# Performance work log

Measured on AMD Instinct MI355X. Metric: run time of the kernel, lower is better.

## Reference

```python
import jax, jax.numpy as jnp
import numpy as np

D_MODEL = 1024
N_HEADS = 16
HEAD_DIM = D_MODEL // N_HEADS
FFN = 4096
NUM_REL = 64
BATCH = 4
SEQ = 1024
EPS = 1e-6


def _layernorm(x, g, b):
    mu = jnp.mean(x, axis=-1, keepdims=True)
    var = jnp.mean(jnp.square(x - mu), axis=-1, keepdims=True)
    return (x - mu) * jax.lax.rsqrt(var + EPS) * g + b


def setup_inputs() -> dict:
    key = jax.random.key(0)
    ks = jax.random.split(key, 16)
    s_d = 1.0 / np.sqrt(D_MODEL)
    s_f = 1.0 / np.sqrt(FFN)
    inp = {
        "x": jax.random.normal(ks[0], (BATCH, SEQ, D_MODEL), jnp.float32),
        "relative_ids": jax.random.randint(ks[1], (SEQ, SEQ), 0, NUM_REL),
        # attention projections (row-major: y = x @ W + b)
        "Wq": jax.random.normal(ks[2], (D_MODEL, D_MODEL), jnp.float32) * s_d,
        "bq": jnp.zeros((D_MODEL,), jnp.float32),
        "Wk": jax.random.normal(ks[3], (D_MODEL, D_MODEL), jnp.float32) * s_d,
        "bk": jnp.zeros((D_MODEL,), jnp.float32),
        "Wv": jax.random.normal(ks[4], (D_MODEL, D_MODEL), jnp.float32) * s_d,
        "bv": jnp.zeros((D_MODEL,), jnp.float32),
        "Wo": jax.random.normal(ks[5], (D_MODEL, D_MODEL), jnp.float32) * s_d,
        "bo": jnp.zeros((D_MODEL,), jnp.float32),
        # relative position tables: Ek for keys (rel-e), Eb per-head bias (rel-b)
        "Ek": jax.random.normal(ks[6], (NUM_REL, HEAD_DIM), jnp.float32) * (1.0 / np.sqrt(HEAD_DIM)),
        "Eb": jax.random.normal(ks[7], (NUM_REL, N_HEADS), jnp.float32) * 0.02,
        # layernorms
        "g1": jnp.ones((D_MODEL,), jnp.float32),
        "b1": jnp.zeros((D_MODEL,), jnp.float32),
        "g2": jnp.ones((D_MODEL,), jnp.float32),
        "b2": jnp.zeros((D_MODEL,), jnp.float32),
        # FFN
        "W1": jax.random.normal(ks[8], (D_MODEL, FFN), jnp.float32) * s_d,
        "bf1": jnp.zeros((FFN,), jnp.float32),
        "W2": jax.random.normal(ks[9], (FFN, D_MODEL), jnp.float32) * s_f,
        "bf2": jnp.zeros((D_MODEL,), jnp.float32),
    }
    return inp


def _forward(x, relative_ids, Wq, bq, Wk, bk, Wv, bv, Wo, bo, Ek, Eb,
             g1, b1, g2, b2, W1, bf1, W2, bf2):
    B, S, D = x.shape
    # projections -> [B, H, S, Dh]
    def split_heads(t):
        return t.reshape(B, S, N_HEADS, HEAD_DIM).transpose(0, 2, 1, 3)
    q = split_heads(x @ Wq + bq)
    k = split_heads(x @ Wk + bk)
    v = split_heads(x @ Wv + bv)

    scores = jnp.einsum('bhqd,bhkd->bhqk', q, k)
    # rel-e: relative key embeddings interact with queries
    Erel = Ek[relative_ids]                      # [S, S, Dh]
    scores = scores + jnp.einsum('bhqd,qkd->bhqk', q, Erel)
    # rel-b: per-head relative bias
    scores = scores + Eb[relative_ids].transpose(2, 0, 1)[None]  # [1,H,S,S]
    scores = scores / jnp.sqrt(jnp.asarray(HEAD_DIM, x.dtype))

    attn = jax.nn.softmax(scores, axis=-1)
    ctx = jnp.einsum('bhqk,bhkd->bhqd', attn, v)
    ctx = ctx.transpose(0, 2, 1, 3).reshape(B, S, D)
    a_out = ctx @ Wo + bo

    # dropout is identity at eval
    ff_in = _layernorm(x + a_out, g1, b1)
    ff = jax.nn.relu(ff_in @ W1 + bf1) @ W2 + bf2
    return _layernorm(ff_in + ff, g2, b2)


def reference(x, relative_ids, Wq, bq, Wk, bk, Wv, bv, Wo, bo, Ek, Eb,
              g1, b1, g2, b2, W1, bf1, W2, bf2):
    return _forward(x, relative_ids, Wq, bq, Wk, bk, Wv, bv, Wo, bo, Ek, Eb,
                    g1, b1, g2, b2, W1, bf1, W2, bf2)
```

## Files before the change

### kernel.cpp

```cpp
#include <hip/hip_runtime.h>


typedef short bf16x8 __attribute__((ext_vector_type(8)));
typedef float f32x4 __attribute__((ext_vector_type(4)));

#define DEVI static __device__ __forceinline__

constexpr int SEQ = 1024, DMODEL = 1024, NH = 16, HDIM = 64, FFDIM = 4096, NREL = 64, NBATCH = 4;
constexpr int ROWS = NBATCH * SEQ;
#define QSC 0.18033688011112042f
#define MAXC 16.0f

DEVI unsigned short f2b(float f) {
  union { float f; unsigned u; } v; v.f = f;
  unsigned r = v.u + 0x7FFFu + ((v.u >> 16) & 1u);
  return (unsigned short)(r >> 16);
}

#if __has_builtin(__builtin_amdgcn_cvt_pk_bf16_f32)
DEVI unsigned pack2(float a, float b) {
  auto r = __builtin_amdgcn_cvt_pk_bf16_f32(a, b);
  return __builtin_bit_cast(unsigned, r);
}
#else
DEVI unsigned pack2(float a, float b) {
  return (unsigned)f2b(a) | ((unsigned)f2b(b) << 16);
}
#endif

DEVI float fexp2(float x) {
#if __has_builtin(__builtin_amdgcn_exp2f)
  return __builtin_amdgcn_exp2f(x);
#else
  return exp2f(x);
#endif
}

DEVI float4 ld4h(const unsigned short* p) {
  uint2 u = *(const uint2*)p;
  union { unsigned v; float f; } a, b, c, d;
  a.v = u.x << 16; b.v = u.x & 0xffff0000u; c.v = u.y << 16; d.v = u.y & 0xffff0000u;
  return make_float4(a.f, b.f, c.f, d.f);
}

DEVI void gload16(const unsigned short* g, unsigned short* l) {
  __builtin_amdgcn_global_load_lds((const __attribute__((address_space(1))) void*)g,
                                   (__attribute__((address_space(3))) void*)l, 16, 0, 0);
}

template <int BM, int BN, int WR, int WC>
DEVI void gemm_core(const unsigned short* __restrict__ A, int lda,
                    const unsigned short* __restrict__ Bt, int ldb, int K,
                    unsigned short* sA, unsigned short* sB, f32x4* acc) {
  constexpr int BK = 64;
  constexpr int MT = BM / (WR * 16), NT = BN / (WC * 16);
  const int tid = threadIdx.x;
  const int wave = tid >> 6, lane = tid & 63;
  const int wm = wave % WR, wn = wave / WR;
  const int lr = lane & 15, kq = lane >> 4;
  const int srow = lane >> 3;
  const int schunk = (lane & 7) ^ (srow & 7);
  const int sw = lr & 7;

  const f32x4 zero = {0.f, 0.f, 0.f, 0.f};
#pragma unroll
  for (int i = 0; i < MT * NT; ++i) acc[i] = zero;

  const unsigned short* ga = A + (size_t)(wave * (BM / 4) + srow) * lda + schunk * 8;
  const unsigned short* gb = Bt + (size_t)(wave * (BN / 4) + srow) * ldb + schunk * 8;
  unsigned short* la = sA + wave * (BM / 4) * BK;
  unsigned short* lb = sB + wave * (BN / 4) * BK;
  const unsigned short* pa = sA + (wm * MT * 16 + lr) * BK;
  const unsigned short* pb = sB + (wn * NT * 16 + lr) * BK;

  for (int k0 = 0; k0 < K; k0 += BK) {
#pragma unroll
    for (int j = 0; j < BM / 32; ++j) gload16(ga + (size_t)(j * 8) * lda + k0, la + j * 8 * BK);
#pragma unroll
    for (int j = 0; j < BN / 32; ++j) gload16(gb + (size_t)(j * 8) * ldb + k0, lb + j * 8 * BK);
    __syncthreads();
#pragma unroll
    for (int ks = 0; ks < 2; ++ks) {
      const int rc = ((ks * 4 + kq) ^ sw) * 8;
      bf16x8 af[MT], bv[NT];
#pragma unroll
      for (int mi = 0; mi < MT; ++mi) af[mi] = *(const bf16x8*)(pa + mi * 16 * BK + rc);
#pragma unroll
      for (int ni = 0; ni < NT; ++ni) bv[ni] = *(const bf16x8*)(pb + ni * 16 * BK + rc);
#pragma unroll
      for (int mi = 0; mi < MT; ++mi)
#pragma unroll
        for (int ni = 0; ni < NT; ++ni)
          acc[mi * NT + ni] =
              __builtin_amdgcn_mfma_f32_16x16x32_bf16(af[mi], bv[ni], acc[mi * NT + ni], 0, 0, 0);
    }
    __syncthreads();
  }
}

#define EPI_VARS                                     \
  const int tid = threadIdx.x;                       \
  const int wave = tid >> 6, lane = tid & 63;        \
  const int wm = wave % WR, wn = wave / WR;          \
  const int lr = lane & 15, kq = lane >> 4;

__global__ __launch_bounds__(256) void k_proj_qkv(
    const unsigned short* __restrict__ A, const unsigned short* __restrict__ WqT,
    const unsigned short* __restrict__ WkT, const unsigned short* __restrict__ WvT,
    const float* __restrict__ bq, const float* __restrict__ bk, const float* __restrict__ bv,
    unsigned short* __restrict__ oq, unsigned short* __restrict__ ok,
    unsigned short* __restrict__ ov) {
  constexpr int BM = 128, BN = 128, WR = 2, WC = 2, MT = 4, NT = 4;
  __shared__ __align__(16) unsigned short sA[BM * 64];
  __shared__ __align__(16) unsigned short sB[BN * 64];
  f32x4 acc[MT * NT];
  const int which = blockIdx.z;
  const unsigned short* Bt = which == 0 ? WqT : which == 1 ? WkT : WvT;
  const float* bias = which == 0 ? bq : which == 1 ? bk : bv;
  unsigned short* out = which == 0 ? oq : which == 1 ? ok : ov;
  const float scl = which == 0 ? QSC : 1.0f;
  const int m0 = blockIdx.y * BM, n0 = blockIdx.x * BN;
  gemm_core<BM, BN, WR, WC>(A + (size_t)m0 * DMODEL, DMODEL, Bt + (size_t)n0 * DMODEL, DMODEL,
                            DMODEL, sA, sB, acc);
  EPI_VARS
#pragma unroll
  for (int mi = 0; mi < MT; ++mi) {
    const int row0 = m0 + wm * MT * 16 + mi * 16 + kq * 4;
    const int b = row0 >> 10, s0 = row0 & 1023;
#pragma unroll
    for (int ni = 0; ni < NT; ++ni) {
      const int col = n0 + wn * NT * 16 + ni * 16 + lr;
      const int h = col >> 6, d = col & 63;
      const float bc = bias[col];
      f32x4 v = acc[mi * NT + ni];
#pragma unroll
      for (int r = 0; r < 4; ++r) v[r] = (v[r] + bc) * scl;
      if (which != 2) {
#pragma unroll
        for (int r = 0; r < 4; ++r)
          out[((size_t)((b * NH + h) * SEQ) + s0 + r) * HDIM + d] = f2b(v[r]);
      } else {
        uint2 p = make_uint2(pack2(v[0], v[1]), pack2(v[2], v[3]));
        *(uint2*)&out[((size_t)((b * NH + h) * HDIM) + d) * SEQ + s0] = p;
      }
    }
  }
}

template <int BM, int BN, int WR, int WC, bool RELU, bool OUTBF16, bool SPLITK = false>
__global__ __launch_bounds__(256) void k_gemm(const unsigned short* __restrict__ A, int lda,
                                              const unsigned short* __restrict__ Bt, int ldb, int K,
                                              int N, const float* __restrict__ bias,
                                              float* __restrict__ outf,
                                              unsigned short* __restrict__ outh,
                                              size_t ostride = 0) {
  constexpr int MT = BM / (WR * 16), NT = BN / (WC * 16);
  __shared__ __align__(16) unsigned short sA[BM * 64];
  __shared__ __align__(16) unsigned short sB[BN * 64];
  f32x4 acc[MT * NT];
  const int m0 = blockIdx.y * BM, n0 = blockIdx.x * BN;
  const int kc = SPLITK ? blockIdx.z : 0;
  gemm_core<BM, BN, WR, WC>(A + (size_t)m0 * lda + (size_t)kc * K, lda,
                            Bt + (size_t)n0 * ldb + (size_t)kc * K, ldb, K, sA, sB, acc);
  if (SPLITK) outh += (size_t)kc * ostride;
  EPI_VARS
#pragma unroll
  for (int mi = 0; mi < MT; ++mi) {
    const int row0 = m0 + wm * MT * 16 + mi * 16 + kq * 4;
#pragma unroll
    for (int ni = 0; ni < NT; ++ni) {
      const int col = n0 + wn * NT * 16 + ni * 16 + lr;
      const float bc = (bias && (!SPLITK || kc == 0)) ? bias[col] : 0.f;
      f32x4 v = acc[mi * NT + ni];
#pragma unroll
      for (int r = 0; r < 4; ++r) {
        float y = v[r] + bc;
        if (RELU) y = fmaxf(y, 0.f);
        if (OUTBF16 || SPLITK)
          outh[(size_t)(row0 + r) * N + col] = f2b(y);
        else
          outf[(size_t)(row0 + r) * N + col] = y;
      }
    }
  }
}

__global__ __launch_bounds__(256) void k_flash(const unsigned short* __restrict__ q,
                                               const unsigned short* __restrict__ kk,
                                               const unsigned short* __restrict__ vT,
                                               const unsigned short* __restrict__ Ekb,
                                               const float* __restrict__ Eb,
                                               const int* __restrict__ rel,
                                               unsigned short* __restrict__ ctx) {
  __shared__ __align__(16) unsigned short sK[128 * 64];
  __shared__ __align__(16) unsigned short sV[64 * 128];
  __shared__ __align__(16) float sqEB[64 * 68];
  __shared__ float sRow[4][16];

  const int tid = threadIdx.x, wave = tid >> 6, lane = tid & 63;
  const int lr = lane & 15, kq = lane >> 4;
  const int qt = blockIdx.x, z = blockIdx.y;
  const int b = z >> 4, h = z & 15;
  const size_t zo = (size_t)z * SEQ * HDIM;
  const size_t vo = (size_t)z * HDIM * SEQ;

  const int srow8 = lane >> 3, sl8 = lane & 7;
  const int sw8 = sl8 ^ (srow8 & 7);
  const int dl = lane >> 4, sl16 = lane & 15;
  const int swl = lr & 7;
  const f32x4 zero = {0.f, 0.f, 0.f, 0.f};

  unsigned short* sQv = sV;
#pragma unroll
  for (int j = 0; j < 2; ++j) {
    const int row = wave * 16 + j * 8 + srow8;
    gload16(q + zo + (size_t)(qt * 64 + row) * 64 + sw8 * 8, sQv + (wave * 16 + j * 8) * 64);
    gload16(Ekb + (size_t)row * 64 + sw8 * 8, sK + (wave * 16 + j * 8) * 64);
  }
  __syncthreads();

  bf16x8 bq_[2];
#pragma unroll
  for (int ks = 0; ks < 2; ++ks)
    bq_[ks] = *(const bf16x8*)&sQv[(wave * 16 + lr) * 64 + (((ks * 4 + kq) ^ swl) << 3)];

  {
    f32x4 accE[4];
#pragma unroll
    for (int nf = 0; nf < 4; ++nf) accE[nf] = zero;
#pragma unroll
    for (int ks = 0; ks < 2; ++ks) {
#pragma unroll
      for (int nf = 0; nf < 4; ++nf) {
        bf16x8 ek = *(const bf16x8*)&sK[(nf * 16 + lr) * 64 + (((ks * 4 + kq) ^ swl) << 3)];
        accE[nf] = __builtin_amdgcn_mfma_f32_16x16x32_bf16(bq_[ks], ek, accE[nf], 0, 0, 0);
      }
    }
#pragma unroll
    for (int nf = 0; nf < 4; ++nf) {
      const int rid = nf * 16 + lr;
      const float eb = Eb[rid * NH + h] * QSC - MAXC;
      f32x4 vv = accE[nf];
      vv[0] += eb; vv[1] += eb; vv[2] += eb; vv[3] += eb;
      *(f32x4*)&sqEB[rid * 68 + wave * 16 + kq * 4] = vv;
    }
  }

  float l_run = 0.f;
  f32x4 accO[4];
#pragma unroll
  for (int nd = 0; nd < 4; ++nd) accO[nd] = zero;
  const int qrow_g = qt * 64 + wave * 16 + lr;
  const int* relrow = rel + (size_t)qrow_g * SEQ;
  const int qcol = wave * 16 + lr;
  unsigned short* sPw = sK + wave * 2048;

  for (int kt = 0; kt < 8; ++kt) {
    __syncthreads();
#pragma unroll
    for (int j = 0; j < 4; ++j) {
      const int row = wave * 32 + j * 8 + srow8;
      gload16(kk + zo + (size_t)(kt * 128 + row) * 64 + sw8 * 8, sK + (wave * 32 + j * 8) * 64);
    }
#pragma unroll
    for (int j = 0; j < 4; ++j) {
      const int row = wave * 16 + j * 4 + dl;
      const int ch = sl16 ^ (row & 15);
      gload16(vT + vo + (size_t)row * SEQ + kt * 128 + ch * 8, sV + (wave * 16 + j * 4) * 128);
    }
    int4 r4[8];
#pragma unroll
    for (int mi = 0; mi < 8; ++mi) r4[mi] = *(const int4*)&relrow[kt * 128 + mi * 16 + kq * 4];
    __syncthreads();

    f32x4 accS[8];
#pragma unroll
    for (int mi = 0; mi < 8; ++mi) accS[mi] = zero;
#pragma unroll
    for (int ks = 0; ks < 2; ++ks) {
#pragma unroll
      for (int mi = 0; mi < 8; ++mi) {
        bf16x8 a = *(const bf16x8*)&sK[(mi * 16 + lr) * 64 + (((ks * 4 + kq) ^ swl) << 3)];
        accS[mi] = __builtin_amdgcn_mfma_f32_16x16x32_bf16(a, bq_[ks], accS[mi], 0, 0, 0);
      }
    }
#pragma unroll
    for (int mi = 0; mi < 8; ++mi) {
      const float p0 = fexp2(accS[mi][0] + sqEB[r4[mi].x * 68 + qcol]);
      const float p1 = fexp2(accS[mi][1] + sqEB[r4[mi].y * 68 + qcol]);
      const float p2 = fexp2(accS[mi][2] + sqEB[r4[mi].z * 68 + qcol]);
      const float p3 = fexp2(accS[mi][3] + sqEB[r4[mi].w * 68 + qcol]);
      accS[mi][0] = p0; accS[mi][1] = p1; accS[mi][2] = p2; accS[mi][3] = p3;
      l_run += (p0 + p1) + (p2 + p3);
    }
    __syncthreads();

#pragma unroll
    for (int mi = 0; mi < 8; ++mi) {
      const int c = 2 * mi + (kq >> 1);
      *(uint2*)&sPw[lr * 128 + ((c ^ lr) << 3) + ((kq & 1) << 2)] =
          make_uint2(pack2(accS[mi][0], accS[mi][1]), pack2(accS[mi][2], accS[mi][3]));
    }
#pragma unroll
    for (int kst = 0; kst < 4; ++kst) {
      const int cc = ((kq + 4 * kst) ^ lr) << 3;
      bf16x8 a = *(const bf16x8*)&sPw[lr * 128 + cc];
#pragma unroll
      for (int nd = 0; nd < 4; ++nd) {
        bf16x8 bv = *(const bf16x8*)&sV[(nd * 16 + lr) * 128 + cc];
        accO[nd] = __builtin_amdgcn_mfma_f32_16x16x32_bf16(a, bv, accO[nd], 0, 0, 0);
      }
    }
  }

  l_run += __shfl_xor(l_run, 16);
  l_run += __shfl_xor(l_run, 32);
  if (kq == 0) sRow[wave][lr] = l_run;
  const float4 lv = *(const float4*)&sRow[wave][kq * 4];
  const float inv[4] = {1.f / lv.x, 1.f / lv.y, 1.f / lv.z, 1.f / lv.w};
  const size_t rbase = (size_t)(b * SEQ + qt * 64 + wave * 16 + kq * 4);
#pragma unroll
  for (int nd = 0; nd < 4; ++nd) {
    const int col = h * HDIM + nd * 16 + lr;
#pragma unroll
    for (int r = 0; r < 4; ++r)
      ctx[(rbase + r) * DMODEL + col] = f2b(accO[nd][r] * inv[r]);
  }
}

template <bool WB>
__global__ __launch_bounds__(256) void k_addln3(const unsigned short* __restrict__ a,
                                                const unsigned short* __restrict__ p0,
                                                const unsigned short* __restrict__ p1,
                                                const float* __restrict__ g,
                                                const float* __restrict__ beta,
                                                float* __restrict__ outf,
                                                unsigned short* __restrict__ outh) {
  const int row = blockIdx.x, t = threadIdx.x;
  const size_t base = (size_t)row * DMODEL + t * 4;
  float4 va = ld4h(&a[base]);
  float4 v0 = ld4h(&p0[base]);
  float4 v1 = ld4h(&p1[base]);
  const float x0 = va.x + v0.x + v1.x, x1 = va.y + v0.y + v1.y;
  const float x2 = va.z + v0.z + v1.z, x3 = va.w + v0.w + v1.w;
  __shared__ float red[4];
  float s = x0 + x1 + x2 + x3;
#pragma unroll
  for (int o = 32; o; o >>= 1) s += __shfl_xor(s, o);
  if ((t & 63) == 0) red[t >> 6] = s;
  __syncthreads();
  const float mu = (red[0] + red[1] + red[2] + red[3]) * (1.0f / DMODEL);
  __syncthreads();
  const float d0 = x0 - mu, d1 = x1 - mu, d2 = x2 - mu, d3 = x3 - mu;
  float qv = d0 * d0 + d1 * d1 + d2 * d2 + d3 * d3;
#pragma unroll
  for (int o = 32; o; o >>= 1) qv += __shfl_xor(qv, o);
  if ((t & 63) == 0) red[t >> 6] = qv;
  __syncthreads();
  const float var = (red[0] + red[1] + red[2] + red[3]) * (1.0f / DMODEL);
  const float sc = rsqrtf(var + 1e-6f);
  float4 vg = *(const float4*)&g[t * 4];
  float4 ve = *(const float4*)&beta[t * 4];
  float4 y;
  y.x = d0 * sc * vg.x + ve.x;
  y.y = d1 * sc * vg.y + ve.y;
  y.z = d2 * sc * vg.z + ve.z;
  y.w = d3 * sc * vg.w + ve.w;
  if (WB) {
    uint2 p = make_uint2(pack2(y.x, y.y), pack2(y.z, y.w));
    *(uint2*)&outh[base] = p;
  } else {
    *(float4*)&outf[base] = y;
  }
}

__global__ __launch_bounds__(256) void k_tcast12(
    const float* __restrict__ Wq, const float* __restrict__ Wk, const float* __restrict__ Wv,
    const float* __restrict__ Wo, const float* __restrict__ W1, const float* __restrict__ W2,
    unsigned short* __restrict__ oq, unsigned short* __restrict__ ok,
    unsigned short* __restrict__ ov, unsigned short* __restrict__ oo,
    unsigned short* __restrict__ o1, unsigned short* __restrict__ o2) {
  const int z = blockIdx.z;
  const float* in;
  unsigned short* out;
  int ldi, ldo;
  if (z < 4) {
    in = z == 0 ? Wq : z == 1 ? Wk : z == 2 ? Wv : Wo;
    out = z == 0 ? oq : z == 1 ? ok : z == 2 ? ov : oo;
    ldi = 1024; ldo = 1024;
  } else if (z < 8) {
    const int s = z - 4;
    in = W1 + (size_t)s * 1024; ldi = 4096;
    out = o1 + (size_t)s * 1024 * 1024; ldo = 1024;
  } else {
    const int s = z - 8;
    in = W2 + (size_t)s * 1024 * 1024; ldi = 1024;
    out = o2 + (size_t)s * 1024; ldo = 4096;
  }
  __shared__ float tile[32][33];
  const int tx = threadIdx.x & 31, ty = threadIdx.x >> 5;
  const int r0 = blockIdx.y * 32, c0 = blockIdx.x * 32;
#pragma unroll
  for (int i = 0; i < 4; ++i)
    tile[ty + i * 8][tx] = in[(size_t)(r0 + ty + i * 8) * ldi + c0 + tx];
  __syncthreads();
#pragma unroll
  for (int i = 0; i < 4; ++i)
    out[(size_t)(c0 + ty + i * 8) * ldo + r0 + tx] = f2b(tile[tx][ty + i * 8]);
}

__global__ __launch_bounds__(256) void k_cast2(const float* __restrict__ a,
                                               unsigned short* __restrict__ oa, int n4a,
                                               const float* __restrict__ bsrc,
                                               unsigned short* __restrict__ ob, int n4b) {
  const int i = blockIdx.x * 256 + threadIdx.x;
  if (i < n4a) {
    float4 v = *(const float4*)&a[(size_t)i * 4];
    uint2 p = make_uint2(pack2(v.x, v.y), pack2(v.z, v.w));
    *(uint2*)&oa[(size_t)i * 4] = p;
  } else {
    const int j = i - n4a;
    if (j < n4b) {
      float4 v = *(const float4*)&bsrc[(size_t)j * 4];
      uint2 p = make_uint2(pack2(v.x, v.y), pack2(v.z, v.w));
      *(uint2*)&ob[(size_t)j * 4] = p;
    }
  }
}


extern "C" void kernel_launch(void* const* d_in, const int* in_sizes, int n_in, void* d_out,
                              int out_size, void* d_ws, size_t ws_size, hipStream_t stream) {
  const float* x = (const float*)d_in[0];
  const int* rel = (const int*)d_in[1];
  const float* Wq = (const float*)d_in[2];
  const float* bq = (const float*)d_in[3];
  const float* Wk = (const float*)d_in[4];
  const float* bk = (const float*)d_in[5];
  const float* Wv = (const float*)d_in[6];
  const float* bv = (const float*)d_in[7];
  const float* Wo = (const float*)d_in[8];
  const float* bo = (const float*)d_in[9];
  const float* Ek = (const float*)d_in[10];
  const float* Eb = (const float*)d_in[11];
  const float* g1 = (const float*)d_in[12];
  const float* b1 = (const float*)d_in[13];
  const float* g2 = (const float*)d_in[14];
  const float* b2 = (const float*)d_in[15];
  const float* W1 = (const float*)d_in[16];
  const float* bf1 = (const float*)d_in[17];
  const float* W2 = (const float*)d_in[18];
  const float* bf2 = (const float*)d_in[19];
  float* out = (float*)d_out;

  char* ws = (char*)d_ws;
  const size_t MB = 1ull << 20;
  unsigned short* Wqt = (unsigned short*)(ws + 0 * MB);
  unsigned short* Wkt = (unsigned short*)(ws + 2 * MB);
  unsigned short* Wvt = (unsigned short*)(ws + 4 * MB);
  unsigned short* Wot = (unsigned short*)(ws + 6 * MB);
  unsigned short* W1t = (unsigned short*)(ws + 8 * MB);
  unsigned short* W2t = (unsigned short*)(ws + 16 * MB);
  unsigned short* xb = (unsigned short*)(ws + 24 * MB);
  unsigned short* Ekb = (unsigned short*)(ws + 32 * MB);
  unsigned short* qbuf = (unsigned short*)(ws + 33 * MB);
  unsigned short* kbuf = (unsigned short*)(ws + 41 * MB);
  unsigned short* vTb = (unsigned short*)(ws + 49 * MB);
  unsigned short* ctx = (unsigned short*)(ws + 57 * MB);
  unsigned short* Pb = (unsigned short*)(ws + 65 * MB);
  unsigned short* ff_in_b = (unsigned short*)(ws + 81 * MB);
  unsigned short* hidden = (unsigned short*)(ws + 89 * MB);
  const size_t OST = (size_t)ROWS * DMODEL;

  k_tcast12<<<dim3(32, 32, 12), 256, 0, stream>>>(Wq, Wk, Wv, Wo, W1, W2, Wqt, Wkt, Wvt, Wot,
                                                  W1t, W2t);
  k_cast2<<<4100, 256, 0, stream>>>(x, xb, ROWS * DMODEL / 4, Ek, Ekb, NREL * HDIM / 4);

  k_proj_qkv<<<dim3(8, 32, 3), 256, 0, stream>>>(xb, Wqt, Wkt, Wvt, bq, bk, bv, qbuf, kbuf, vTb);

  k_flash<<<dim3(16, 64), 256, 0, stream>>>(qbuf, kbuf, vTb, Ekb, Eb, rel, ctx);

  k_gemm<128, 128, 2, 2, false, true, true><<<dim3(8, 32, 2), 256, 0, stream>>>(
      ctx, DMODEL, Wot, DMODEL, DMODEL / 2, DMODEL, bo, nullptr, Pb, OST);
  k_addln3<true><<<ROWS, 256, 0, stream>>>(xb, Pb, Pb + OST, g1, b1, nullptr, ff_in_b);

  k_gemm<128, 128, 2, 2, true, true><<<dim3(32, 32), 256, 0, stream>>>(
      ff_in_b, DMODEL, W1t, DMODEL, DMODEL, FFDIM, bf1, nullptr, hidden);
  k_gemm<128, 128, 2, 2, false, true, true><<<dim3(8, 32, 2), 256, 0, stream>>>(
      hidden, FFDIM, W2t, FFDIM, FFDIM / 2, DMODEL, bf2, nullptr, Pb, OST);
  k_addln3<false><<<ROWS, 256, 0, stream>>>(ff_in_b, Pb, Pb + OST, g2, b2, out, nullptr);
}
```

Baseline: 382.7 us.

## Stream K/V directly from global in flash kernel, compress relative ids to bytes

```diff
diff --git a/kernel.cpp b/kernel.cpp
--- a/kernel.cpp
+++ b/kernel.cpp
@@ -185,44 +185,34 @@
   }
 }
 
-__global__ __launch_bounds__(256) void k_flash(const unsigned short* __restrict__ q,
-                                               const unsigned short* __restrict__ kk,
-                                               const unsigned short* __restrict__ vT,
-                                               const unsigned short* __restrict__ Ekb,
-                                               const float* __restrict__ Eb,
-                                               const int* __restrict__ rel,
-                                               unsigned short* __restrict__ ctx) {
-  __shared__ __align__(16) unsigned short sK[128 * 64];
-  __shared__ __align__(16) unsigned short sV[64 * 128];
-  __shared__ __align__(16) float sqEB[64 * 68];
+__global__ __launch_bounds__(256, 4) void k_flash(const unsigned short* __restrict__ q,
+                                                  const unsigned short* __restrict__ kk,
+                                                  const unsigned short* __restrict__ vT,
+                                                  const unsigned short* __restrict__ Ekb,
+                                                  const float* __restrict__ Eb,
+                                                  const unsigned char* __restrict__ rel8,
+                                                  unsigned short* __restrict__ ctx) {
+  __shared__ __align__(16) float sqEB[64 * 65];
+  __shared__ __align__(16) unsigned short sP[4 * 2048];
   __shared__ float sRow[4][16];
 
   const int tid = threadIdx.x, wave = tid >> 6, lane = tid & 63;
   const int lr = lane & 15, kq = lane >> 4;
-  const int qt = blockIdx.x, z = blockIdx.y;
+
+  const int L = blockIdx.y * 16 + blockIdx.x;
+  const int xcd = L & 7, idx = L >> 3;
+  const int z = xcd * 8 + (idx >> 4), qt = idx & 15;
   const int b = z >> 4, h = z & 15;
   const size_t zo = (size_t)z * SEQ * HDIM;
   const size_t vo = (size_t)z * HDIM * SEQ;
 
-  const int srow8 = lane >> 3, sl8 = lane & 7;
-  const int sw8 = sl8 ^ (srow8 & 7);
-  const int dl = lane >> 4, sl16 = lane & 15;
-  const int swl = lr & 7;
   const f32x4 zero = {0.f, 0.f, 0.f, 0.f};
 
-  unsigned short* sQv = sV;
-#pragma unroll
-  for (int j = 0; j < 2; ++j) {
-    const int row = wave * 16 + j * 8 + srow8;
-    gload16(q + zo + (size_t)(qt * 64 + row) * 64 + sw8 * 8, sQv + (wave * 16 + j * 8) * 64);
-    gload16(Ekb + (size_t)row * 64 + sw8 * 8, sK + (wave * 16 + j * 8) * 64);
-  }
-  __syncthreads();
-
+  const int qrow_g = qt * 64 + wave * 16 + lr;
   bf16x8 bq_[2];
 #pragma unroll
   for (int ks = 0; ks < 2; ++ks)
-    bq_[ks] = *(const bf16x8*)&sQv[(wave * 16 + lr) * 64 + (((ks * 4 + kq) ^ swl) << 3)];
+    bq_[ks] = *(const bf16x8*)&q[zo + (size_t)qrow_g * HDIM + ((ks * 4 + kq) << 3)];
 
   {
     f32x4 accE[4];
@@ -232,7 +222,7 @@
     for (int ks = 0; ks < 2; ++ks) {
 #pragma unroll
       for (int nf = 0; nf < 4; ++nf) {
-        bf16x8 ek = *(const bf16x8*)&sK[(nf * 16 + lr) * 64 + (((ks * 4 + kq) ^ swl) << 3)];
+        bf16x8 ek = *(const bf16x8*)&Ekb[(nf * 16 + lr) * HDIM + ((ks * 4 + kq) << 3)];
         accE[nf] = __builtin_amdgcn_mfma_f32_16x16x32_bf16(bq_[ks], ek, accE[nf], 0, 0, 0);
       }
     }
@@ -240,9 +230,9 @@
     for (int nf = 0; nf < 4; ++nf) {
       const int rid = nf * 16 + lr;
       const float eb = Eb[rid * NH + h] * QSC - MAXC;
-      f32x4 vv = accE[nf];
-      vv[0] += eb; vv[1] += eb; vv[2] += eb; vv[3] += eb;
-      *(f32x4*)&sqEB[rid * 68 + wave * 16 + kq * 4] = vv;
+      const int base = rid * 65 + wave * 16 + kq * 4;
+#pragma unroll
+      for (int r = 0; r < 4; ++r) sqEB[base + r] = accE[nf][r] + eb;
     }
   }
 
@@ -250,29 +240,17 @@
   f32x4 accO[4];
 #pragma unroll
   for (int nd = 0; nd < 4; ++nd) accO[nd] = zero;
-  const int qrow_g = qt * 64 + wave * 16 + lr;
-  const int* relrow = rel + (size_t)qrow_g * SEQ;
+  const unsigned char* relrow8 = rel8 + (size_t)qrow_g * SEQ;
   const int qcol = wave * 16 + lr;
-  unsigned short* sPw = sK + wave * 2048;
+  unsigned short* sPw = sP + wave * 2048;
 
   for (int kt = 0; kt < 8; ++kt) {
-    __syncthreads();
-#pragma unroll
-    for (int j = 0; j < 4; ++j) {
-      const int row = wave * 32 + j * 8 + srow8;
-      gload16(kk + zo + (size_t)(kt * 128 + row) * 64 + sw8 * 8, sK + (wave * 32 + j * 8) * 64);
-    }
-#pragma unroll
-    for (int j = 0; j < 4; ++j) {
-      const int row = wave * 16 + j * 4 + dl;
-      const int ch = sl16 ^ (row & 15);
-      gload16(vT + vo + (size_t)row * SEQ + kt * 128 + ch * 8, sV + (wave * 16 + j * 4) * 128);
-    }
-    int4 r4[8];
-#pragma unroll
-    for (int mi = 0; mi < 8; ++mi) r4[mi] = *(const int4*)&relrow[kt * 128 + mi * 16 + kq * 4];
-    __syncthreads();
-
+    unsigned ru[8];
+#pragma unroll
+    for (int mi = 0; mi < 8; ++mi)
+      ru[mi] = *(const unsigned*)&relrow8[kt * 128 + mi * 16 + kq * 4];
+
+    const unsigned short* kbase = kk + zo + (size_t)(kt * 128) * HDIM;
     f32x4 accS[8];
 #pragma unroll
     for (int mi = 0; mi < 8; ++mi) accS[mi] = zero;
@@ -280,34 +258,34 @@
     for (int ks = 0; ks < 2; ++ks) {
 #pragma unroll
       for (int mi = 0; mi < 8; ++mi) {
-        bf16x8 a = *(const bf16x8*)&sK[(mi * 16 + lr) * 64 + (((ks * 4 + kq) ^ swl) << 3)];
+        bf16x8 a = *(const bf16x8*)&kbase[(mi * 16 + lr) * HDIM + ((ks * 4 + kq) << 3)];
         accS[mi] = __builtin_amdgcn_mfma_f32_16x16x32_bf16(a, bq_[ks], accS[mi], 0, 0, 0);
       }
     }
 #pragma unroll
     for (int mi = 0; mi < 8; ++mi) {
-      const float p0 = fexp2(accS[mi][0] + sqEB[r4[mi].x * 68 + qcol]);
-      const float p1 = fexp2(accS[mi][1] + sqEB[r4[mi].y * 68 + qcol]);
-      const float p2 = fexp2(accS[mi][2] + sqEB[r4[mi].z * 68 + qcol]);
-      const float p3 = fexp2(accS[mi][3] + sqEB[r4[mi].w * 68 + qcol]);
+      const float p0 = fexp2(accS[mi][0] + sqEB[(int)(ru[mi] & 255u) * 65 + qcol]);
+      const float p1 = fexp2(accS[mi][1] + sqEB[(int)((ru[mi] >> 8) & 255u) * 65 + qcol]);
+      const float p2 = fexp2(accS[mi][2] + sqEB[(int)((ru[mi] >> 16) & 255u) * 65 + qcol]);
+      const float p3 = fexp2(accS[mi][3] + sqEB[(int)(ru[mi] >> 24) * 65 + qcol]);
       accS[mi][0] = p0; accS[mi][1] = p1; accS[mi][2] = p2; accS[mi][3] = p3;
       l_run += (p0 + p1) + (p2 + p3);
     }
-    __syncthreads();
-
 #pragma unroll
     for (int mi = 0; mi < 8; ++mi) {
       const int c = 2 * mi + (kq >> 1);
       *(uint2*)&sPw[lr * 128 + ((c ^ lr) << 3) + ((kq & 1) << 2)] =
           make_uint2(pack2(accS[mi][0], accS[mi][1]), pack2(accS[mi][2], accS[mi][3]));
     }
+    const unsigned short* vbase = vT + vo + kt * 128;
 #pragma unroll
     for (int kst = 0; kst < 4; ++kst) {
       const int cc = ((kq + 4 * kst) ^ lr) << 3;
       bf16x8 a = *(const bf16x8*)&sPw[lr * 128 + cc];
+      const int kc = (kst * 4 + kq) << 3;
 #pragma unroll
       for (int nd = 0; nd < 4; ++nd) {
-        bf16x8 bv = *(const bf16x8*)&sV[(nd * 16 + lr) * 128 + cc];
+        bf16x8 bv = *(const bf16x8*)&vbase[(size_t)(nd * 16 + lr) * SEQ + kc];
         accO[nd] = __builtin_amdgcn_mfma_f32_16x16x32_bf16(a, bv, accO[nd], 0, 0, 0);
       }
     }
@@ -412,7 +390,9 @@
 __global__ __launch_bounds__(256) void k_cast2(const float* __restrict__ a,
                                                unsigned short* __restrict__ oa, int n4a,
                                                const float* __restrict__ bsrc,
-                                               unsigned short* __restrict__ ob, int n4b) {
+                                               unsigned short* __restrict__ ob, int n4b,
+                                               const int* __restrict__ rel,
+                                               unsigned char* __restrict__ r8, int n4c) {
   const int i = blockIdx.x * 256 + threadIdx.x;
   if (i < n4a) {
     float4 v = *(const float4*)&a[(size_t)i * 4];
@@ -424,6 +404,14 @@
       float4 v = *(const float4*)&bsrc[(size_t)j * 4];
       uint2 p = make_uint2(pack2(v.x, v.y), pack2(v.z, v.w));
       *(uint2*)&ob[(size_t)j * 4] = p;
+    } else {
+      const int k2 = j - n4b;
+      if (k2 < n4c) {
+        int4 v = *(const int4*)&rel[(size_t)k2 * 4];
+        unsigned pk = (unsigned)(v.x & 255) | ((unsigned)(v.y & 255) << 8) |
+                      ((unsigned)(v.z & 255) << 16) | ((unsigned)(v.w & 255) << 24);
+        *(unsigned*)&r8[(size_t)k2 * 4] = pk;
+      }
     }
   }
 }
@@ -468,17 +456,19 @@
   unsigned short* vTb = (unsigned short*)(ws + 49 * MB);
   unsigned short* ctx = (unsigned short*)(ws + 57 * MB);
   unsigned short* Pb = (unsigned short*)(ws + 65 * MB);
+  unsigned char* rel8 = (unsigned char*)(ws + 65 * MB);
   unsigned short* ff_in_b = (unsigned short*)(ws + 81 * MB);
   unsigned short* hidden = (unsigned short*)(ws + 89 * MB);
   const size_t OST = (size_t)ROWS * DMODEL;
 
   k_tcast12<<<dim3(32, 32, 12), 256, 0, stream>>>(Wq, Wk, Wv, Wo, W1, W2, Wqt, Wkt, Wvt, Wot,
                                                   W1t, W2t);
-  k_cast2<<<4100, 256, 0, stream>>>(x, xb, ROWS * DMODEL / 4, Ek, Ekb, NREL * HDIM / 4);
+  k_cast2<<<5124, 256, 0, stream>>>(x, xb, ROWS * DMODEL / 4, Ek, Ekb, NREL * HDIM / 4, rel, rel8,
+                                    SEQ * SEQ / 4);
 
   k_proj_qkv<<<dim3(8, 32, 3), 256, 0, stream>>>(xb, Wqt, Wkt, Wvt, bq, bk, bv, qbuf, kbuf, vTb);
 
-  k_flash<<<dim3(16, 64), 256, 0, stream>>>(qbuf, kbuf, vTb, Ekb, Eb, rel, ctx);
+  k_flash<<<dim3(16, 64), 256, 0, stream>>>(qbuf, kbuf, vTb, Ekb, Eb, rel8, ctx);
 
   k_gemm<128, 128, 2, 2, false, true, true><<<dim3(8, 32, 2), 256, 0, stream>>>(
       ctx, DMODEL, Wot, DMODEL, DMODEL / 2, DMODEL, bo, nullptr, Pb, OST);
```

Result: slower. 472.5 us (+23.5%).

## Prefetch K/V tiles into registers, pack relative ids to bytes, remap flash blocks

Applied to the files above, without the earlier changes.

```diff
diff --git a/kernel.cpp b/kernel.cpp
--- a/kernel.cpp
+++ b/kernel.cpp
@@ -185,13 +185,13 @@
   }
 }
 
-__global__ __launch_bounds__(256) void k_flash(const unsigned short* __restrict__ q,
-                                               const unsigned short* __restrict__ kk,
-                                               const unsigned short* __restrict__ vT,
-                                               const unsigned short* __restrict__ Ekb,
-                                               const float* __restrict__ Eb,
-                                               const int* __restrict__ rel,
-                                               unsigned short* __restrict__ ctx) {
+__global__ __launch_bounds__(256, 3) void k_flash(const unsigned short* __restrict__ q,
+                                                  const unsigned short* __restrict__ kk,
+                                                  const unsigned short* __restrict__ vT,
+                                                  const unsigned short* __restrict__ Ekb,
+                                                  const float* __restrict__ Eb,
+                                                  const unsigned char* __restrict__ rel8,
+                                                  unsigned short* __restrict__ ctx) {
   __shared__ __align__(16) unsigned short sK[128 * 64];
   __shared__ __align__(16) unsigned short sV[64 * 128];
   __shared__ __align__(16) float sqEB[64 * 68];
@@ -199,7 +199,10 @@
 
   const int tid = threadIdx.x, wave = tid >> 6, lane = tid & 63;
   const int lr = lane & 15, kq = lane >> 4;
-  const int qt = blockIdx.x, z = blockIdx.y;
+
+  const int L = blockIdx.y * 16 + blockIdx.x;
+  const int xcd = L & 7, idx = L >> 3;
+  const int z = xcd * 8 + (idx >> 4), qt = idx & 15;
   const int b = z >> 4, h = z & 15;
   const size_t zo = (size_t)z * SEQ * HDIM;
   const size_t vo = (size_t)z * HDIM * SEQ;
@@ -223,6 +226,15 @@
 #pragma unroll
   for (int ks = 0; ks < 2; ++ks)
     bq_[ks] = *(const bf16x8*)&sQv[(wave * 16 + lr) * 64 + (((ks * 4 + kq) ^ swl) << 3)];
+
+  const unsigned short* kg = kk + zo + (size_t)(wave * 32 + srow8) * 64 + sw8 * 8;
+  uint4 kreg[4], vreg[4];
+#pragma unroll
+  for (int j = 0; j < 4; ++j) kreg[j] = *(const uint4*)(kg + j * 512);
+#pragma unroll
+  for (int j = 0; j < 4; ++j)
+    vreg[j] = *(const uint4*)(vT + vo + (size_t)(wave * 16 + j * 4 + dl) * SEQ +
+                              (sl16 ^ (j * 4 + dl)) * 8);
 
   {
     f32x4 accE[4];
@@ -251,26 +263,22 @@
 #pragma unroll
   for (int nd = 0; nd < 4; ++nd) accO[nd] = zero;
   const int qrow_g = qt * 64 + wave * 16 + lr;
-  const int* relrow = rel + (size_t)qrow_g * SEQ;
+  const unsigned char* relrow8 = rel8 + (size_t)qrow_g * SEQ;
   const int qcol = wave * 16 + lr;
   unsigned short* sPw = sK + wave * 2048;
 
   for (int kt = 0; kt < 8; ++kt) {
     __syncthreads();
 #pragma unroll
-    for (int j = 0; j < 4; ++j) {
-      const int row = wave * 32 + j * 8 + srow8;
-      gload16(kk + zo + (size_t)(kt * 128 + row) * 64 + sw8 * 8, sK + (wave * 32 + j * 8) * 64);
-    }
-#pragma unroll
-    for (int j = 0; j < 4; ++j) {
-      const int row = wave * 16 + j * 4 + dl;
-      const int ch = sl16 ^ (row & 15);
-      gload16(vT + vo + (size_t)row * SEQ + kt * 128 + ch * 8, sV + (wave * 16 + j * 4) * 128);
-    }
-    int4 r4[8];
-#pragma unroll
-    for (int mi = 0; mi < 8; ++mi) r4[mi] = *(const int4*)&relrow[kt * 128 + mi * 16 + kq * 4];
+    for (int j = 0; j < 4; ++j)
+      *(uint4*)(sK + (size_t)(wave * 32 + j * 8 + srow8) * 64 + sl8 * 8) = kreg[j];
+#pragma unroll
+    for (int j = 0; j < 4; ++j)
+      *(uint4*)(sV + (size_t)(wave * 16 + j * 4 + dl) * 128 + sl16 * 8) = vreg[j];
+    unsigned ru[8];
+#pragma unroll
+    for (int mi = 0; mi < 8; ++mi)
+      ru[mi] = *(const unsigned*)&relrow8[kt * 128 + mi * 16 + kq * 4];
     __syncthreads();
 
     f32x4 accS[8];
@@ -286,14 +294,24 @@
     }
 #pragma unroll
     for (int mi = 0; mi < 8; ++mi) {
-      const float p0 = fexp2(accS[mi][0] + sqEB[r4[mi].x * 68 + qcol]);
-      const float p1 = fexp2(accS[mi][1] + sqEB[r4[mi].y * 68 + qcol]);
-      const float p2 = fexp2(accS[mi][2] + sqEB[r4[mi].z * 68 + qcol]);
-      const float p3 = fexp2(accS[mi][3] + sqEB[r4[mi].w * 68 + qcol]);
+      const float p0 = fexp2(accS[mi][0] + sqEB[(int)(ru[mi] & 255u) * 68 + qcol]);
+      const float p1 = fexp2(accS[mi][1] + sqEB[(int)((ru[mi] >> 8) & 255u) * 68 + qcol]);
+      const float p2 = fexp2(accS[mi][2] + sqEB[(int)((ru[mi] >> 16) & 255u) * 68 + qcol]);
+      const float p3 = fexp2(accS[mi][3] + sqEB[(int)(ru[mi] >> 24) * 68 + qcol]);
       accS[mi][0] = p0; accS[mi][1] = p1; accS[mi][2] = p2; accS[mi][3] = p3;
       l_run += (p0 + p1) + (p2 + p3);
     }
     __syncthreads();
+
+    if (kt < 7) {
+      const unsigned short* kgn = kg + (size_t)(kt + 1) * 8192;
+#pragma unroll
+      for (int j = 0; j < 4; ++j) kreg[j] = *(const uint4*)(kgn + j * 512);
+#pragma unroll
+      for (int j = 0; j < 4; ++j)
+        vreg[j] = *(const uint4*)(vT + vo + (size_t)(wave * 16 + j * 4 + dl) * SEQ +
+                                  (kt + 1) * 128 + (sl16 ^ (j * 4 + dl)) * 8);
+    }
 
 #pragma unroll
     for (int mi = 0; mi < 8; ++mi) {
@@ -412,7 +430,9 @@
 __global__ __launch_bounds__(256) void k_cast2(const float* __restrict__ a,
                                                unsigned short* __restrict__ oa, int n4a,
                                                const float* __restrict__ bsrc,
-                                               unsigned short* __restrict__ ob, int n4b) {
+                                               unsigned short* __restrict__ ob, int n4b,
+                                               const int* __restrict__ rel,
+                                               unsigned char* __restrict__ r8, int n4c) {
   const int i = blockIdx.x * 256 + threadIdx.x;
   if (i < n4a) {
     float4 v = *(const float4*)&a[(size_t)i * 4];
@@ -424,6 +444,14 @@
       float4 v = *(const float4*)&bsrc[(size_t)j * 4];
       uint2 p = make_uint2(pack2(v.x, v.y), pack2(v.z, v.w));
       *(uint2*)&ob[(size_t)j * 4] = p;
+    } else {
+      const int k2 = j - n4b;
+      if (k2 < n4c) {
+        int4 v = *(const int4*)&rel[(size_t)k2 * 4];
+        unsigned pk = (unsigned)(v.x & 255) | ((unsigned)(v.y & 255) << 8) |
+                      ((unsigned)(v.z & 255) << 16) | ((unsigned)(v.w & 255) << 24);
+        *(unsigned*)&r8[(size_t)k2 * 4] = pk;
+      }
     }
   }
 }
@@ -468,17 +496,19 @@
   unsigned short* vTb = (unsigned short*)(ws + 49 * MB);
   unsigned short* ctx = (unsigned short*)(ws + 57 * MB);
   unsigned short* Pb = (unsigned short*)(ws + 65 * MB);
+  unsigned char* rel8 = (unsigned char*)(ws + 65 * MB);
   unsigned short* ff_in_b = (unsigned short*)(ws + 81 * MB);
   unsigned short* hidden = (unsigned short*)(ws + 89 * MB);
   const size_t OST = (size_t)ROWS * DMODEL;
 
   k_tcast12<<<dim3(32, 32, 12), 256, 0, stream>>>(Wq, Wk, Wv, Wo, W1, W2, Wqt, Wkt, Wvt, Wot,
                                                   W1t, W2t);
-  k_cast2<<<4100, 256, 0, stream>>>(x, xb, ROWS * DMODEL / 4, Ek, Ekb, NREL * HDIM / 4);
+  k_cast2<<<5124, 256, 0, stream>>>(x, xb, ROWS * DMODEL / 4, Ek, Ekb, NREL * HDIM / 4, rel, rel8,
+                                    SEQ * SEQ / 4);
 
   k_proj_qkv<<<dim3(8, 32, 3), 256, 0, stream>>>(xb, Wqt, Wkt, Wvt, bq, bk, bv, qbuf, kbuf, vTb);
 
-  k_flash<<<dim3(16, 64), 256, 0, stream>>>(qbuf, kbuf, vTb, Ekb, Eb, rel, ctx);
+  k_flash<<<dim3(16, 64), 256, 0, stream>>>(qbuf, kbuf, vTb, Ekb, Eb, rel8, ctx);
 
   k_gemm<128, 128, 2, 2, false, true, true><<<dim3(8, 32, 2), 256, 0, stream>>>(
       ctx, DMODEL, Wot, DMODEL, DMODEL / 2, DMODEL, bo, nullptr, Pb, OST);
```

After: 428.2 us. 1.12x slower.
